# Optimization experiments

Hardware: AMD Instinct MI355X
Metric: run time of the kernel (lower is better)

## Reference

```python
import jax, jax.numpy as jnp
import numpy as np

H, W, C = 192, 192, 1024

def setup_inputs() -> dict:
    key = jax.random.key(0)
    k1, k2 = jax.random.split(key)
    x = jax.random.normal(k1, (1, H, W, C), dtype=jnp.float32)
    gamma = jax.random.normal(k2, (1,), dtype=jnp.float32)
    return {"x": x, "gamma": gamma}

def reference(x, gamma):
    b, h, w, c = x.shape
    # NOTE: faithful to the TF code: a pure reshape of NHWC into (1, C, H*W),
    # with NO transpose (the original relies on reshape semantics).
    proj = x.reshape(1, c, h * w)                      # query == key^T == value
    energy = jnp.einsum('bcn,bdn->bcd', proj, proj)    # (1, C, C)
    energy_new = jnp.max(energy, axis=-1, keepdims=True) - energy  # sign-flipped
    attention = jax.nn.softmax(energy_new, axis=-1)    # (1, C, C)
    out = jnp.einsum('bcd,bdn->bcn', attention, proj)  # (1, C, H*W)
    out = out.reshape(1, h, w, c)
    return gamma * out + x
```

## Files before the change

kernel.cpp:

```cpp
#include <hip/hip_runtime.h>
#include <cstdint>

#define C_DIM 1024
#define N_DIM 36864

typedef unsigned short ushort_t;
typedef __attribute__((ext_vector_type(8))) short bf16x8;
typedef __attribute__((ext_vector_type(4))) float f32x4;

__device__ __forceinline__ ushort_t f2b(float f) {
    unsigned u = __float_as_uint(f);
    u = (u + 0x7fffu + ((u >> 16) & 1u)) >> 16;
    return (ushort_t)u;
}
__device__ __forceinline__ float b2f(ushort_t b) {
    return __uint_as_float(((unsigned)b) << 16);
}

__device__ __forceinline__ void async16(const void* g, const void* lds) {
    __builtin_amdgcn_global_load_lds(
        (const __attribute__((address_space(1))) unsigned int*)(uintptr_t)g,
        (__attribute__((address_space(3))) unsigned int*)(uint32_t)(uintptr_t)lds,
        16, 0, 0);
}


__global__ __launch_bounds__(256) void k_convert(const float* __restrict__ x,
                                                 ushort_t* __restrict__ ph,
                                                 ushort_t* __restrict__ pl) {
    int i = blockIdx.x * 256 + threadIdx.x;
    float4 v = ((const float4*)x)[i];
    ushort4 h, l;
    h.x = f2b(v.x); l.x = f2b(v.x - b2f(h.x));
    h.y = f2b(v.y); l.y = f2b(v.y - b2f(h.y));
    h.z = f2b(v.z); l.z = f2b(v.z - b2f(h.z));
    h.w = f2b(v.w); l.w = f2b(v.w - b2f(h.w));
    ((ushort4*)ph)[i] = h;
    ((ushort4*)pl)[i] = l;
}

__global__ __launch_bounds__(256) void k_convtrans(const float* __restrict__ x,
                                                   ushort_t* __restrict__ ph,
                                                   ushort_t* __restrict__ pl,
                                                   ushort_t* __restrict__ pht) {
    __shared__ __align__(16) ushort_t th[64][72];
    const int t = threadIdx.x;
    const int i = t >> 2, qd = t & 3;
    const int c0 = blockIdx.y << 6;
    const size_t n0 = (size_t)blockIdx.x << 6;

    const size_t row = (size_t)(c0 + i) * N_DIM + n0 + (qd << 4);
    const float* src = x + row;
    union { ushort_t s[16]; uint4 q[2]; } H, Lo;
#pragma unroll
    for (int u4 = 0; u4 < 4; ++u4) {
        float4 v = ((const float4*)src)[u4];
        ushort_t h0 = f2b(v.x), h1 = f2b(v.y), h2 = f2b(v.z), h3 = f2b(v.w);
        H.s[u4 * 4 + 0] = h0; Lo.s[u4 * 4 + 0] = f2b(v.x - b2f(h0));
        H.s[u4 * 4 + 1] = h1; Lo.s[u4 * 4 + 1] = f2b(v.y - b2f(h1));
        H.s[u4 * 4 + 2] = h2; Lo.s[u4 * 4 + 2] = f2b(v.z - b2f(h2));
        H.s[u4 * 4 + 3] = h3; Lo.s[u4 * 4 + 3] = f2b(v.w - b2f(h3));
    }
    *(uint4*)(ph + row)     = H.q[0];
    *(uint4*)(ph + row + 8) = H.q[1];
    *(uint4*)(pl + row)     = Lo.q[0];
    *(uint4*)(pl + row + 8) = Lo.q[1];
    *(uint4*)&th[i][qd << 4]       = H.q[0];
    *(uint4*)&th[i][(qd << 4) + 8] = H.q[1];
    __syncthreads();

    ushort_t tmp[16];
#pragma unroll
    for (int u = 0; u < 16; ++u) tmp[u] = th[(qd << 4) + u][i];
    ushort_t* dst = pht + (n0 + i) * C_DIM + c0 + (qd << 4);
    *(uint4*)dst       = *(uint4*)tmp;
    *(uint4*)(dst + 8) = *(uint4*)(tmp + 8);
}

__global__ __launch_bounds__(256, 2) void k_egemm(const ushort_t* __restrict__ ph,
                                                  const ushort_t* __restrict__ pl,
                                                  float* __restrict__ g1,
                                                  float* __restrict__ g2,
                                                  int kchunk) {
    __shared__ __align__(16) ushort_t sAh[2][128 * 32];
    __shared__ __align__(16) ushort_t sAl[2][128 * 32];
    __shared__ __align__(16) ushort_t sBh[2][128 * 32];
    __shared__ __align__(16) ushort_t sBl[2][128 * 32];

    const int t = threadIdx.x;
    const int w = t >> 6;
    const int L = t & 63;

    int pr = blockIdx.x, pi = 0;
    while (pr >= 8 - pi) { pr -= 8 - pi; ++pi; }
    const int c0 = pi << 7;
    const int d0 = (pi + pr) << 7;

    const int kb = blockIdx.z * kchunk;
    const int lrow = L >> 2;
    const int lcol = (((L & 3) ^ ((L >> 3) & 3)) << 3);

    const size_t rA = (size_t)(c0 + (w << 5) + lrow) * N_DIM + kb + lcol;
    const size_t rB = (size_t)(d0 + (w << 5) + lrow) * N_DIM + kb + lcol;
    const ushort_t* gAh = ph + rA;
    const ushort_t* gAl = pl + rA;
    const ushort_t* gBh = ph + rB;
    const ushort_t* gBl = pl + rB;
    const int wb = w << 10;

    const int wm = (w >> 1) << 6;
    const int wn = (w & 1) << 6;
    const int lm = L & 15, q = L >> 4;
    const int co = ((q ^ ((lm >> 1) & 3)) << 3);

    f32x4 acc1[4][4], acc2[4][4];
#pragma unroll
    for (int a = 0; a < 4; ++a)
#pragma unroll
        for (int b = 0; b < 4; ++b) { acc1[a][b] = (f32x4)0.0f; acc2[a][b] = (f32x4)0.0f; }

    auto stage = [&](int ti, int b) {
        const int o = ti << 5;
        async16(gAh + o,              sAh[b] + wb);
        async16(gAh + o + 16 * N_DIM, sAh[b] + wb + 512);
        async16(gAl + o,              sAl[b] + wb);
        async16(gAl + o + 16 * N_DIM, sAl[b] + wb + 512);
        async16(gBh + o,              sBh[b] + wb);
        async16(gBh + o + 16 * N_DIM, sBh[b] + wb + 512);
        async16(gBl + o,              sBl[b] + wb);
        async16(gBl + o + 16 * N_DIM, sBl[b] + wb + 512);
    };

    const int nIter = kchunk >> 5;
    stage(0, 0);

    for (int ti = 0; ti < nIter; ++ti) {
        const int cb = ti & 1;
        if (ti + 1 < nIter) {
            stage(ti + 1, cb ^ 1);
            __builtin_amdgcn_s_waitcnt(0x0F78);
        } else {
            __builtin_amdgcn_s_waitcnt(0x0F70);
        }
        __builtin_amdgcn_s_barrier();

        bf16x8 ah[4], al[4], bh[4], bl[4];
#pragma unroll
        for (int mt = 0; mt < 4; ++mt) {
            const int ro = ((wm + (mt << 4) + lm) << 5) + co;
            ah[mt] = *(const bf16x8*)(sAh[cb] + ro);
            al[mt] = *(const bf16x8*)(sAl[cb] + ro);
        }
#pragma unroll
        for (int nt = 0; nt < 4; ++nt) {
            const int ro = ((wn + (nt << 4) + lm) << 5) + co;
            bh[nt] = *(const bf16x8*)(sBh[cb] + ro);
            bl[nt] = *(const bf16x8*)(sBl[cb] + ro);
        }
#pragma unroll
        for (int mt = 0; mt < 4; ++mt)
#pragma unroll
            for (int nt = 0; nt < 4; ++nt) {
                acc1[mt][nt] = __builtin_amdgcn_mfma_f32_16x16x32_bf16(ah[mt], bh[nt], acc1[mt][nt], 0, 0, 0);
                acc2[mt][nt] = __builtin_amdgcn_mfma_f32_16x16x32_bf16(ah[mt], bl[nt], acc2[mt][nt], 0, 0, 0);
                acc2[mt][nt] = __builtin_amdgcn_mfma_f32_16x16x32_bf16(al[mt], bh[nt], acc2[mt][nt], 0, 0, 0);
            }
        __builtin_amdgcn_s_barrier();
    }

    const size_t base = ((size_t)blockIdx.z * 36 + blockIdx.x) << 14;
#pragma unroll
    for (int mt = 0; mt < 4; ++mt)
#pragma unroll
        for (int nt = 0; nt < 4; ++nt)
#pragma unroll
            for (int r = 0; r < 4; ++r) {
                int lr = wm + (mt << 4) + (q << 2) + r;
                int lc = wn + (nt << 4) + lm;
                size_t o = base + ((size_t)lr << 7) + lc;
                g1[o] = acc1[mt][nt][r];
                g2[o] = acc2[mt][nt][r];
            }
}

__global__ __launch_bounds__(256) void k_reduce(const float* __restrict__ g1,
                                                const float* __restrict__ g2,
                                                float* __restrict__ E,
                                                int splitk) {
    __shared__ float ld[64][65];
    const int t = threadIdx.x;
    const int i = t >> 2;
    const int jb = (t & 3) << 4;

    int pr = blockIdx.x, ci = 0;
    while (pr >= 16 - ci) { pr -= 16 - ci; ++ci; }
    const int cb = ci, db = ci + pr;
    const int i8 = cb >> 1, j8 = db >> 1;
    const int p = i8 * (17 - i8) / 2 + (j8 - i8);
    const size_t tbase = ((size_t)p << 14) + ((size_t)(cb & 1) << 13) + ((size_t)(db & 1) << 6);

    float acc[16];
#pragma unroll
    for (int u = 0; u < 16; ++u) acc[u] = 0.0f;

    for (int z = 0; z < splitk; ++z) {
        const size_t zo = (size_t)z * (36 << 14) + tbase + ((size_t)i << 7) + jb;
        const float* p1 = g1 + zo;
        const float* p2 = g2 + zo;
#pragma unroll
        for (int u4 = 0; u4 < 4; ++u4) {
            float4 v1 = ((const float4*)p1)[u4];
            float4 v2 = ((const float4*)p2)[u4];
            acc[u4 * 4 + 0] += v1.x + v2.x;
            acc[u4 * 4 + 1] += v1.y + v2.y;
            acc[u4 * 4 + 2] += v1.z + v2.z;
            acc[u4 * 4 + 3] += v1.w + v2.w;
        }
    }

    float* eo = E + ((size_t)((cb << 6) + i) << 10) + (db << 6) + jb;
#pragma unroll
    for (int u4 = 0; u4 < 4; ++u4) {
        float4 v;
        v.x = acc[u4 * 4 + 0]; v.y = acc[u4 * 4 + 1];
        v.z = acc[u4 * 4 + 2]; v.w = acc[u4 * 4 + 3];
        ((float4*)eo)[u4] = v;
    }

    if (cb != db) {
#pragma unroll
        for (int u4 = 0; u4 < 4; ++u4)
            *(float4*)&ld[i][jb + u4 * 4] = *(float4*)&acc[u4 * 4];
        __syncthreads();
        float tmp[16];
#pragma unroll
        for (int u = 0; u < 16; ++u) tmp[u] = ld[jb + u][i];
        float* et = E + ((size_t)((db << 6) + i) << 10) + (cb << 6) + jb;
#pragma unroll
        for (int u4 = 0; u4 < 4; ++u4)
            ((float4*)et)[u4] = *(float4*)&tmp[u4 * 4];
    }
}

__global__ __launch_bounds__(256) void k_softmax(const float* __restrict__ E,
                                                 ushort_t* __restrict__ att) {
    const int c = blockIdx.x;
    const int t = threadIdx.x;
    __shared__ float red[4];
    __shared__ float bcast;

    float4 e4 = ((const float4*)E)[((size_t)c << 8) + t];
    float m = fminf(fminf(e4.x, e4.y), fminf(e4.z, e4.w));
#pragma unroll
    for (int off = 32; off > 0; off >>= 1) m = fminf(m, __shfl_down(m, off));
    if ((t & 63) == 0) red[t >> 6] = m;
    __syncthreads();
    if (t == 0) bcast = fminf(fminf(red[0], red[1]), fminf(red[2], red[3]));
    __syncthreads();
    m = bcast;

    float w0 = expf(m - e4.x), w1 = expf(m - e4.y);
    float w2 = expf(m - e4.z), w3 = expf(m - e4.w);
    float s = w0 + w1 + w2 + w3;
#pragma unroll
    for (int off = 32; off > 0; off >>= 1) s += __shfl_down(s, off);
    if ((t & 63) == 0) red[t >> 6] = s;
    __syncthreads();
    if (t == 0) bcast = red[0] + red[1] + red[2] + red[3];
    __syncthreads();
    float inv = 1.0f / bcast;
    ushort4 o;
    o.x = f2b(w0 * inv); o.y = f2b(w1 * inv);
    o.z = f2b(w2 * inv); o.w = f2b(w3 * inv);
    ((ushort4*)att)[((size_t)c << 8) + t] = o;
}

__global__ __launch_bounds__(256) void k_transpose(const ushort_t* __restrict__ ph,
                                                   ushort_t* __restrict__ pht) {
    __shared__ __align__(16) ushort_t tile[64][72];
    const int t = threadIdx.x;
    const int i = t >> 2, qd = t & 3;
    const int c0 = blockIdx.y << 6;
    const size_t n0 = (size_t)blockIdx.x << 6;

    const ushort_t* src = ph + (size_t)(c0 + i) * N_DIM + n0 + (qd << 4);
    uint4 v0 = *(const uint4*)src;
    uint4 v1 = *(const uint4*)(src + 8);
    *(uint4*)&tile[i][qd << 4]       = v0;
    *(uint4*)&tile[i][(qd << 4) + 8] = v1;
    __syncthreads();

    ushort_t tmp[16];
#pragma unroll
    for (int u = 0; u < 16; ++u) tmp[u] = tile[(qd << 4) + u][i];
    ushort_t* dst = pht + (n0 + i) * C_DIM + c0 + (qd << 4);
    *(uint4*)dst       = *(uint4*)tmp;
    *(uint4*)(dst + 8) = *(uint4*)(tmp + 8);
}

__global__ __launch_bounds__(256) void k_ogemm(const ushort_t* __restrict__ att,
                                               const ushort_t* __restrict__ pht,
                                               const float* __restrict__ x,
                                               const float* __restrict__ gamma,
                                               float* __restrict__ out) {
    __shared__ __align__(16) ushort_t sA[2][128 * 32];
    __shared__ __align__(16) ushort_t sB[2][128 * 32];

    const int t = threadIdx.x;
    const int w = t >> 6, L = t & 63;
    const int n0 = blockIdx.x << 7;
    const int c0 = blockIdx.y << 7;
    const int srow = L >> 2;
    const int scol = (((L & 3) ^ ((L >> 3) & 3)) << 3);

    const int wm = (w >> 1) << 6, wn = (w & 1) << 6;
    const int lm = L & 15, q = L >> 4;
    const int co = ((q ^ ((lm >> 1) & 3)) << 3);

    f32x4 acc[4][4];
#pragma unroll
    for (int a = 0; a < 4; ++a)
#pragma unroll
        for (int b = 0; b < 4; ++b) acc[a][b] = (f32x4)0.0f;

    auto stage = [&](int k0, int b) {
#pragma unroll
        for (int j = 0; j < 4; ++j) {
            int ch = (w << 2) + j;
            int row = ((ch & 7) << 4) + srow;
            const ushort_t* src = (ch < 8)
                ? att + (size_t)(c0 + row) * C_DIM + k0 + scol
                : pht + (size_t)(n0 + row) * C_DIM + k0 + scol;
            ushort_t* base = (ch < 8) ? sA[b] : sB[b];
            async16(src, base + (((ch & 7) << 4) << 5));
        }
    };

    const int nIter = C_DIM / 32;
    stage(0, 0);

    for (int ti = 0; ti < nIter; ++ti) {
        const int cb = ti & 1;
        if (ti + 1 < nIter) {
            stage((ti + 1) << 5, cb ^ 1);
            __builtin_amdgcn_s_waitcnt(0x0F74);
        } else {
            __builtin_amdgcn_s_waitcnt(0x0F70);
        }
        __builtin_amdgcn_s_barrier();

        bf16x8 a[4], b[4];
#pragma unroll
        for (int mt = 0; mt < 4; ++mt)
            a[mt] = *(const bf16x8*)(sA[cb] + ((wm + (mt << 4) + lm) << 5) + co);
#pragma unroll
        for (int nt = 0; nt < 4; ++nt)
            b[nt] = *(const bf16x8*)(sB[cb] + ((wn + (nt << 4) + lm) << 5) + co);
#pragma unroll
        for (int mt = 0; mt < 4; ++mt)
#pragma unroll
            for (int nt = 0; nt < 4; ++nt)
                acc[mt][nt] = __builtin_amdgcn_mfma_f32_16x16x32_bf16(a[mt], b[nt], acc[mt][nt], 0, 0, 0);
        __builtin_amdgcn_s_barrier();
    }

    const float g = gamma[0];
#pragma unroll
    for (int mt = 0; mt < 4; ++mt)
#pragma unroll
        for (int nt = 0; nt < 4; ++nt)
#pragma unroll
            for (int r = 0; r < 4; ++r) {
                int cg = c0 + wm + (mt << 4) + (q << 2) + r;
                int ng = n0 + wn + (nt << 4) + lm;
                size_t o = (size_t)cg * N_DIM + ng;
                out[o] = g * acc[mt][nt][r] + x[o];
            }
}

extern "C" void kernel_launch(void* const* d_in, const int* in_sizes, int n_in,
                              void* d_out, int out_size, void* d_ws, size_t ws_size,
                              hipStream_t stream) {
    const float* x     = (const float*)d_in[0];
    const float* gamma = (const float*)d_in[1];
    float* out = (float*)d_out;
    char* ws = (char*)d_ws;

    const size_t P  = 75497472ull;
    const size_t GT = 2359296ull;
    const size_t EB = 4194304ull, AT = 2097152ull;

    auto need = [&](int s, bool f) {
        return (size_t)(f ? 3 : 2) * P + (size_t)s * 2 * GT + EB + AT;
    };

    int S = 12;
    bool fused = true;
    if (ws_size < need(12, true)) {
        if      (ws_size >= need(8, true)) S = 8;
        else if (ws_size >= need(4, true)) S = 4;
        else {
            fused = false; S = 12;
            if (ws_size < need(12, false)) S = 8;
            if (ws_size < need(8,  false)) S = 4;
        }
    }
    const int kchunk = N_DIM / S;

    if (fused) {
        ushort_t* ph  = (ushort_t*)(ws);
        ushort_t* pl  = (ushort_t*)(ws + P);
        ushort_t* pht = (ushort_t*)(ws + 2 * P);
        float*    g1  = (float*)   (ws + 3 * P);
        float*    g2  = (float*)   (ws + 3 * P + (size_t)S * GT);
        float*    E   = (float*)   (ws + 3 * P + (size_t)S * 2 * GT);
        ushort_t* att = (ushort_t*)(ws + 3 * P + (size_t)S * 2 * GT + EB);

        k_convtrans<<<dim3(N_DIM / 64, C_DIM / 64), 256, 0, stream>>>(x, ph, pl, pht);
        k_egemm<<<dim3(36, 1, S), 256, 0, stream>>>(ph, pl, g1, g2, kchunk);
        k_reduce<<<dim3(136), 256, 0, stream>>>(g1, g2, E, S);
        k_softmax<<<dim3(C_DIM), 256, 0, stream>>>(E, att);
        k_ogemm<<<dim3(N_DIM / 128, C_DIM / 128), 256, 0, stream>>>(att, pht, x, gamma, out);
    } else {
        ushort_t* ph  = (ushort_t*)(ws);
        ushort_t* pl  = (ushort_t*)(ws + P);
        float*    g1  = (float*)   (ws + 2 * P);
        float*    g2  = (float*)   (ws + 2 * P + (size_t)S * GT);
        float*    E   = (float*)   (ws + 2 * P + (size_t)S * 2 * GT);
        ushort_t* att = (ushort_t*)(ws + 2 * P + (size_t)S * 2 * GT + EB);
        ushort_t* pht = pl;

        k_convert<<<dim3((C_DIM * (size_t)N_DIM / 4) / 256), 256, 0, stream>>>(x, ph, pl);
        k_egemm<<<dim3(36, 1, S), 256, 0, stream>>>(ph, pl, g1, g2, kchunk);
        k_reduce<<<dim3(136), 256, 0, stream>>>(g1, g2, E, S);
        k_softmax<<<dim3(C_DIM), 256, 0, stream>>>(E, att);
        k_transpose<<<dim3(N_DIM / 64, C_DIM / 64), 256, 0, stream>>>(ph, pht);
        k_ogemm<<<dim3(N_DIM / 128, C_DIM / 128), 256, 0, stream>>>(att, pht, x, gamma, out);
    }
}
```

Baseline: 628.4 us.

## Remap GEMM blocks across XCDs and widen output GEMM tile to 128x256

The energy GEMM now uses a flat 1D grid with an XCD-aware mapping. Each XCD chunk gets a consistent set of upper-triangle tiles and K-splits, with padding blocks that return early, so tiles sharing inputs are more likely to land on the same L2. The output GEMM tile grows from 128x128 to 128x256: each wave computes 4x8 MFMA tiles, staging widens to 6 async chunks per wave, and the waitcnt is adjusted to match. Blocks are ordered so that consecutive N tiles map to the same XCD. This aims to reuse the attention tile across more columns and improve L2 locality, at the cost of more registers and LDS per block and a launch bound of 2 blocks per CU.

```diff
diff --git a/kernel.cpp b/kernel.cpp
--- a/kernel.cpp
+++ b/kernel.cpp
@@ -87,16 +87,25 @@
     __shared__ __align__(16) ushort_t sBh[2][128 * 32];
     __shared__ __align__(16) ushort_t sBl[2][128 * 32];
 
-    const int t = threadIdx.x;
-    const int w = t >> 6;
-    const int L = t & 63;
-
-    int pr = blockIdx.x, pi = 0;
+    const int f   = blockIdx.x;
+    const int xcd = f & 7;
+    const int r   = f >> 3;
+    const int z   = r / 5;
+    const int s   = r - z * 5;
+    const int chunk = (xcd + ((z & 1) << 2)) & 7;
+    if (chunk >= 4 && s == 4) return;
+    const int u = (chunk < 4) ? (chunk * 5 + s) : (20 + (chunk - 4) * 4 + s);
+
+    int pr = u, pi = 0;
     while (pr >= 8 - pi) { pr -= 8 - pi; ++pi; }
     const int c0 = pi << 7;
     const int d0 = (pi + pr) << 7;
 
-    const int kb = blockIdx.z * kchunk;
+    const int t = threadIdx.x;
+    const int w = t >> 6;
+    const int L = t & 63;
+
+    const int kb = z * kchunk;
     const int lrow = L >> 2;
     const int lcol = (((L & 3) ^ ((L >> 3) & 3)) << 3);
 
@@ -168,18 +177,18 @@
         __builtin_amdgcn_s_barrier();
     }
 
-    const size_t base = ((size_t)blockIdx.z * 36 + blockIdx.x) << 14;
+    const size_t base = ((size_t)z * 36 + u) << 14;
 #pragma unroll
     for (int mt = 0; mt < 4; ++mt)
 #pragma unroll
         for (int nt = 0; nt < 4; ++nt)
 #pragma unroll
-            for (int r = 0; r < 4; ++r) {
-                int lr = wm + (mt << 4) + (q << 2) + r;
+            for (int r2 = 0; r2 < 4; ++r2) {
+                int lr = wm + (mt << 4) + (q << 2) + r2;
                 int lc = wn + (nt << 4) + lm;
                 size_t o = base + ((size_t)lr << 7) + lc;
-                g1[o] = acc1[mt][nt][r];
-                g2[o] = acc2[mt][nt][r];
+                g1[o] = acc1[mt][nt][r2];
+                g2[o] = acc2[mt][nt][r2];
             }
 }
 
@@ -298,41 +307,53 @@
     *(uint4*)(dst + 8) = *(uint4*)(tmp + 8);
 }
 
-__global__ __launch_bounds__(256) void k_ogemm(const ushort_t* __restrict__ att,
-                                               const ushort_t* __restrict__ pht,
-                                               const float* __restrict__ x,
-                                               const float* __restrict__ gamma,
-                                               float* __restrict__ out) {
+__global__ __launch_bounds__(256, 2) void k_ogemm(const ushort_t* __restrict__ att,
+                                                  const ushort_t* __restrict__ pht,
+                                                  const float* __restrict__ x,
+                                                  const float* __restrict__ gamma,
+                                                  float* __restrict__ out) {
     __shared__ __align__(16) ushort_t sA[2][128 * 32];
-    __shared__ __align__(16) ushort_t sB[2][128 * 32];
+    __shared__ __align__(16) ushort_t sB[2][256 * 32];
+
+    const int d   = blockIdx.x;
+    const int xcd = d & 7;
+    const int r   = d >> 3;
+    const int a0  = r >> 3;
+    const int cbk = r & 7;
+    const int n0 = (xcd * 18 + a0) << 8;
+    const int c0 = cbk << 7;
 
     const int t = threadIdx.x;
     const int w = t >> 6, L = t & 63;
-    const int n0 = blockIdx.x << 7;
-    const int c0 = blockIdx.y << 7;
     const int srow = L >> 2;
     const int scol = (((L & 3) ^ ((L >> 3) & 3)) << 3);
 
-    const int wm = (w >> 1) << 6, wn = (w & 1) << 6;
+    const int wm = (w >> 1) << 6;
+    const int wn = (w & 1) << 7;
     const int lm = L & 15, q = L >> 4;
     const int co = ((q ^ ((lm >> 1) & 3)) << 3);
 
-    f32x4 acc[4][4];
+    f32x4 acc[4][8];
 #pragma unroll
     for (int a = 0; a < 4; ++a)
 #pragma unroll
-        for (int b = 0; b < 4; ++b) acc[a][b] = (f32x4)0.0f;
+        for (int b = 0; b < 8; ++b) acc[a][b] = (f32x4)0.0f;
 
     auto stage = [&](int k0, int b) {
 #pragma unroll
-        for (int j = 0; j < 4; ++j) {
-            int ch = (w << 2) + j;
-            int row = ((ch & 7) << 4) + srow;
-            const ushort_t* src = (ch < 8)
-                ? att + (size_t)(c0 + row) * C_DIM + k0 + scol
-                : pht + (size_t)(n0 + row) * C_DIM + k0 + scol;
-            ushort_t* base = (ch < 8) ? sA[b] : sB[b];
-            async16(src, base + (((ch & 7) << 4) << 5));
+        for (int j = 0; j < 6; ++j) {
+            int ch = w * 6 + j;
+            const ushort_t* src;
+            ushort_t* base;
+            if (ch < 8) {
+                src = att + (size_t)(c0 + (ch << 4) + srow) * C_DIM + k0 + scol;
+                base = sA[b] + (ch << 9);
+            } else {
+                int rb = ch - 8;
+                src = pht + (size_t)(n0 + (rb << 4) + srow) * C_DIM + k0 + scol;
+                base = sB[b] + (rb << 9);
+            }
+            async16(src, base);
         }
     };
 
@@ -343,23 +364,23 @@
         const int cb = ti & 1;
         if (ti + 1 < nIter) {
             stage((ti + 1) << 5, cb ^ 1);
-            __builtin_amdgcn_s_waitcnt(0x0F74);
+            __builtin_amdgcn_s_waitcnt(0x0F76);
         } else {
             __builtin_amdgcn_s_waitcnt(0x0F70);
         }
         __builtin_amdgcn_s_barrier();
 
-        bf16x8 a[4], b[4];
+        bf16x8 a[4], b[8];
 #pragma unroll
         for (int mt = 0; mt < 4; ++mt)
             a[mt] = *(const bf16x8*)(sA[cb] + ((wm + (mt << 4) + lm) << 5) + co);
 #pragma unroll
-        for (int nt = 0; nt < 4; ++nt)
+        for (int nt = 0; nt < 8; ++nt)
             b[nt] = *(const bf16x8*)(sB[cb] + ((wn + (nt << 4) + lm) << 5) + co);
 #pragma unroll
         for (int mt = 0; mt < 4; ++mt)
 #pragma unroll
-            for (int nt = 0; nt < 4; ++nt)
+            for (int nt = 0; nt < 8; ++nt)
                 acc[mt][nt] = __builtin_amdgcn_mfma_f32_16x16x32_bf16(a[mt], b[nt], acc[mt][nt], 0, 0, 0);
         __builtin_amdgcn_s_barrier();
     }
@@ -368,13 +389,13 @@
 #pragma unroll
     for (int mt = 0; mt < 4; ++mt)
 #pragma unroll
-        for (int nt = 0; nt < 4; ++nt)
-#pragma unroll
-            for (int r = 0; r < 4; ++r) {
-                int cg = c0 + wm + (mt << 4) + (q << 2) + r;
+        for (int nt = 0; nt < 8; ++nt)
+#pragma unroll
+            for (int r2 = 0; r2 < 4; ++r2) {
+                int cg = c0 + wm + (mt << 4) + (q << 2) + r2;
                 int ng = n0 + wn + (nt << 4) + lm;
                 size_t o = (size_t)cg * N_DIM + ng;
-                out[o] = g * acc[mt][nt][r] + x[o];
+                out[o] = g * acc[mt][nt][r2] + x[o];
             }
 }
 
@@ -417,10 +438,10 @@
         ushort_t* att = (ushort_t*)(ws + 3 * P + (size_t)S * 2 * GT + EB);
 
         k_convtrans<<<dim3(N_DIM / 64, C_DIM / 64), 256, 0, stream>>>(x, ph, pl, pht);
-        k_egemm<<<dim3(36, 1, S), 256, 0, stream>>>(ph, pl, g1, g2, kchunk);
+        k_egemm<<<dim3(40 * S), 256, 0, stream>>>(ph, pl, g1, g2, kchunk);
         k_reduce<<<dim3(136), 256, 0, stream>>>(g1, g2, E, S);
         k_softmax<<<dim3(C_DIM), 256, 0, stream>>>(E, att);
-        k_ogemm<<<dim3(N_DIM / 128, C_DIM / 128), 256, 0, stream>>>(att, pht, x, gamma, out);
+        k_ogemm<<<dim3(1152), 256, 0, stream>>>(att, pht, x, gamma, out);
     } else {
         ushort_t* ph  = (ushort_t*)(ws);
         ushort_t* pl  = (ushort_t*)(ws + P);
@@ -431,10 +452,10 @@
         ushort_t* pht = pl;
 
         k_convert<<<dim3((C_DIM * (size_t)N_DIM / 4) / 256), 256, 0, stream>>>(x, ph, pl);
-        k_egemm<<<dim3(36, 1, S), 256, 0, stream>>>(ph, pl, g1, g2, kchunk);
+        k_egemm<<<dim3(40 * S), 256, 0, stream>>>(ph, pl, g1, g2, kchunk);
         k_reduce<<<dim3(136), 256, 0, stream>>>(g1, g2, E, S);
         k_softmax<<<dim3(C_DIM), 256, 0, stream>>>(E, att);
         k_transpose<<<dim3(N_DIM / 64, C_DIM / 64), 256, 0, stream>>>(ph, pht);
-        k_ogemm<<<dim3(N_DIM / 128, C_DIM / 128), 256, 0, stream>>>(att, pht, x, gamma, out);
-    }
-}
+        k_ogemm<<<dim3(1152), 256, 0, stream>>>(att, pht, x, gamma, out);
+    }
+}
```

Result: faster. 585.0 us (-6.9%).
